# Optimization experiments

Hardware: AMD Instinct MI355X
Metric: run time of the kernel (lower is better)

The kernel has to match this reference:

```python
import jax, jax.numpy as jnp
import numpy as np

B, T, C = 4, 1024, 1024
N_HEAD = 16
MEMORY = 64  # sliding-window size: key j visible to query i iff 0 <= i-j <= MEMORY


def setup_inputs() -> dict:
    key = jax.random.key(0)
    k1, k2, k3 = jax.random.split(key, 3)
    x = jax.random.normal(k1, (B, T, C), dtype=jnp.float32)
    # torch Linear weight is [out, in]; we store transposed [in, out] for x @ W
    W_attn = jax.random.normal(k2, (C, 3 * C), dtype=jnp.float32) * (1.0 / np.sqrt(C))
    W_proj = jax.random.normal(k3, (C, C), dtype=jnp.float32) * (1.0 / np.sqrt(C))
    return {"x": x, "W_attn": W_attn, "W_proj": W_proj}


def reference(x, W_attn, W_proj):
    Bv, Tv, Cv = x.shape
    hd = Cv // N_HEAD
    qkv = x @ W_attn                               # [B,T,3C]
    q, k, v = jnp.split(qkv, 3, axis=-1)
    def heads(t):
        return t.reshape(Bv, Tv, N_HEAD, hd).transpose(0, 2, 1, 3)  # [B,H,T,hd]
    q, k, v = heads(q), heads(k), heads(v)
    scale = 1.0 / np.sqrt(hd)
    scores = jnp.einsum('bhqd,bhkd->bhqk', q, k) * scale            # [B,H,T,T]
    i = jnp.arange(Tv)
    diff = i[:, None] - i[None, :]                                  # i - j
    band_mask = (diff >= 0) & (diff <= MEMORY)                      # M1 * ~M2
    y = jax.nn.softmax(jnp.where(band_mask, scores, -jnp.inf), axis=-1) @ v
    # get_att=True path: full causal attention probabilities (no window)
    att = jax.nn.softmax(jnp.where(diff >= 0, scores, -jnp.inf), axis=-1)
    att_std = jnp.std(att, axis=0, ddof=1)                          # torch .std default ddof=1
    y = y.transpose(0, 2, 1, 3).reshape(Bv, Tv, Cv)
    y = y @ W_proj
    return (y, att, att_std)
```

## Files before the change

kernel.cpp:

```cpp
#include <hip/hip_runtime.h>
#include <hip/hip_bf16.h>
#include <stdint.h>

#define Bb 4
#define Tt 1024
#define Hh 16
#define HD 64
#define C3 3072
#define WIN 64

typedef __bf16 bf16x8 __attribute__((ext_vector_type(8)));
typedef float f32x4 __attribute__((ext_vector_type(4)));

#define MFMA16(a, b, c) __builtin_amdgcn_mfma_f32_16x16x32_bf16((a), (b), (c), 0, 0, 0)

static __device__ __forceinline__ unsigned short f2bf(float f) {
  union { float f; unsigned u; } v; v.f = f;
  unsigned r = (v.u + 0x7FFFu + ((v.u >> 16) & 1u)) >> 16;
  return (unsigned short)r;
}
static __device__ __forceinline__ float bf2f(unsigned short h) {
  union { unsigned u; float f; } v; v.u = ((unsigned)h) << 16;
  return v.f;
}

__global__ __launch_bounds__(256) void k_prep(const float* __restrict__ x,
                                              const float* __restrict__ Wa,
                                              const float* __restrict__ Wp,
                                              unsigned short* __restrict__ xbf,
                                              unsigned short* __restrict__ WtA,
                                              unsigned short* __restrict__ WtP) {
  __shared__ float tile[32][33];
  const int blk = blockIdx.x;
  const int tid = threadIdx.x;
  if (blk < 4096) {
    int i = blk * 256 + tid;
    float4 v = ((const float4*)x)[i];
    ushort4 o;
    o.x = f2bf(v.x); o.y = f2bf(v.y); o.z = f2bf(v.z); o.w = f2bf(v.w);
    ((ushort4*)xbf)[i] = o;
    return;
  }
  const float* Win; unsigned short* Wt; int N, n0, k0;
  if (blk < 7168) { int bb = blk - 4096; Win = Wa; Wt = WtA; N = 3072; n0 = (bb % 96) * 32; k0 = (bb / 96) * 32; }
  else           { int bb = blk - 7168; Win = Wp; Wt = WtP; N = 1024; n0 = (bb % 32) * 32; k0 = (bb / 32) * 32; }
  const int K = 1024;
  int tx = tid & 31, ty = tid >> 5;
  for (int r = ty; r < 32; r += 8)
    tile[r][tx] = Win[(size_t)(k0 + r) * N + n0 + tx];
  __syncthreads();
  for (int r = ty; r < 32; r += 8)
    Wt[(size_t)(n0 + r) * K + k0 + tx] = f2bf(tile[tx][r]);
}

template <int BM, int BF16_OUT, int SCALEQ>
__global__ __launch_bounds__(256) void k_gemm_bt(const unsigned short* __restrict__ A,
                                                 const unsigned short* __restrict__ Bt,
                                                 void* __restrict__ Cv, int M, int N, int K) {
  constexpr int MI = BM / 32;
  __shared__ unsigned short lds[BM * 32 + 128 * 32];
  unsigned short* as_ = lds;
  unsigned short* bs_ = lds + BM * 32;
  const int tid = threadIdx.x;
  const int m0 = blockIdx.x * BM, n0 = blockIdx.y * 128;
  const int w = tid >> 6, lane = tid & 63;
  const int wm = (w >> 1) * (BM / 2), wn = (w & 1) * 64;
  const int lrow = lane & 15, lk = lane >> 4;

  f32x4 z = {0.f, 0.f, 0.f, 0.f};
  f32x4 acc[MI][4];
#pragma unroll
  for (int i = 0; i < MI; ++i)
#pragma unroll
    for (int j = 0; j < 4; ++j) acc[i][j] = z;

  const int nk = K >> 5;
  for (int kt = 0; kt < nk; ++kt) {
    const int k0 = kt << 5;
    __syncthreads();
#pragma unroll
    for (int p = 0; p < BM / 64; ++p) {
      int seg = tid + p * 256;
      int row = seg >> 2, ks = (seg & 3) << 3;
      __builtin_amdgcn_global_load_lds(
          (__attribute__((address_space(1))) void*)(A + (size_t)(m0 + row) * K + k0 + ks),
          (__attribute__((address_space(3))) void*)(as_ + seg * 8), 16, 0, 0);
    }
#pragma unroll
    for (int p = 0; p < 2; ++p) {
      int seg = tid + p * 256;
      int row = seg >> 2, ks = (seg & 3) << 3;
      __builtin_amdgcn_global_load_lds(
          (__attribute__((address_space(1))) void*)(Bt + (size_t)(n0 + row) * K + k0 + ks),
          (__attribute__((address_space(3))) void*)(bs_ + seg * 8), 16, 0, 0);
    }
    __syncthreads();
    bf16x8 af[MI], bfr[4];
#pragma unroll
    for (int f = 0; f < MI; ++f)
      af[f] = *(const bf16x8*)(as_ + (wm + f * 16 + lrow) * 32 + lk * 8);
#pragma unroll
    for (int f = 0; f < 4; ++f)
      bfr[f] = *(const bf16x8*)(bs_ + (wn + f * 16 + lrow) * 32 + lk * 8);
#pragma unroll
    for (int i = 0; i < MI; ++i)
#pragma unroll
      for (int j = 0; j < 4; ++j) acc[i][j] = MFMA16(af[i], bfr[j], acc[i][j]);
  }
  const int r0 = lk * 4;
#pragma unroll
  for (int i = 0; i < MI; ++i)
#pragma unroll
    for (int j = 0; j < 4; ++j)
#pragma unroll
      for (int r = 0; r < 4; ++r) {
        int gm = m0 + wm + i * 16 + r0 + r;
        int gn = n0 + wn + j * 16 + lrow;
        float v = acc[i][j][r];
        if (SCALEQ) {
          if (gn < 1024) v *= 0.125f;
        }
        if (BF16_OUT)
          ((unsigned short*)Cv)[(size_t)gm * N + gn] = f2bf(v);
        else
          ((float*)Cv)[(size_t)gm * N + gn] = v;
      }
}

__global__ __launch_bounds__(512) void k_att(const unsigned short* __restrict__ qkv,
                                             float* __restrict__ att, float* __restrict__ astd) {
  const int x = blockIdx.x;
  const int ti = (x & 1) ? (x >> 1) : (31 - (x >> 1));
  const int h = blockIdx.y;
  const int i0 = ti * 32;
  const int tid = threadIdx.x;
  const int w = tid >> 6, lane = tid & 63;
  const int lrow = lane & 15, lk = lane >> 4;

  __shared__ float smrh[2][4][32];
  __shared__ float smr[4][32];
  __shared__ float wbuf[2][8][32][36];

  {
    const int b1 = w & 3, half = w >> 2;
    const size_t qb_ = ((size_t)(b1 * Tt + i0 + lrow)) * C3 + h * 64 + lk * 8;
    bf16x8 q00 = *(const bf16x8*)(qkv + qb_);
    bf16x8 q01 = *(const bf16x8*)(qkv + qb_ + 32);
    bf16x8 q10 = *(const bf16x8*)(qkv + qb_ + (size_t)16 * C3);
    bf16x8 q11 = *(const bf16x8*)(qkv + qb_ + (size_t)16 * C3 + 32);

    float l[2][4];
#pragma unroll
    for (int i2 = 0; i2 < 2; ++i2)
#pragma unroll
      for (int r = 0; r < 4; ++r) l[i2][r] = 0.f;

    for (int jt = half; jt <= ti; jt += 2) {
      const int j0 = jt * 32;
      const size_t krowa = ((size_t)(b1 * Tt + j0 + lrow)) * C3 + 1024 + h * 64 + lk * 8;
      const size_t krowb = krowa + (size_t)16 * C3;
      bf16x8 k00 = *(const bf16x8*)(qkv + krowa);
      bf16x8 k01 = *(const bf16x8*)(qkv + krowa + 32);
      bf16x8 k10 = *(const bf16x8*)(qkv + krowb);
      bf16x8 k11 = *(const bf16x8*)(qkv + krowb + 32);
      const int ja = j0 + lrow, jb2 = j0 + 16 + lrow;
#pragma unroll
      for (int i2 = 0; i2 < 2; ++i2) {
        bf16x8 qa = i2 ? q10 : q00;
        bf16x8 qb = i2 ? q11 : q01;
        f32x4 sa = {0.f, 0.f, 0.f, 0.f}, sb = {0.f, 0.f, 0.f, 0.f};
        sa = MFMA16(qa, k00, sa);
        sa = MFMA16(qb, k01, sa);
        sb = MFMA16(qa, k10, sb);
        sb = MFMA16(qb, k11, sb);
#pragma unroll
        for (int r = 0; r < 4; ++r) {
          int ig = i0 + i2 * 16 + lk * 4 + r;
          float pa = (ja <= ig) ? __expf(sa[r]) : 0.f;
          float pb = (jb2 <= ig) ? __expf(sb[r]) : 0.f;
          l[i2][r] += pa + pb;
        }
      }
    }
#pragma unroll
    for (int i2 = 0; i2 < 2; ++i2)
#pragma unroll
      for (int r = 0; r < 4; ++r) {
        float ll = l[i2][r];
#pragma unroll
        for (int d = 1; d <= 8; d <<= 1) ll += __shfl_xor(ll, d);
        if (lrow == 0) smrh[half][b1][i2 * 16 + lk * 4 + r] = ll;
      }
  }
  __syncthreads();
  if (tid < 128) {
    int b = tid >> 5, row = tid & 31;
    smr[b][row] = 1.0f / (smrh[0][b][row] + smrh[1][b][row]);
  }
  __syncthreads();

  bf16x8 qf[4][2][2];
#pragma unroll
  for (int b = 0; b < 4; ++b) {
    const size_t qb_ = ((size_t)(b * Tt + i0 + lrow)) * C3 + h * 64 + lk * 8;
    qf[b][0][0] = *(const bf16x8*)(qkv + qb_);
    qf[b][0][1] = *(const bf16x8*)(qkv + qb_ + 32);
    qf[b][1][0] = *(const bf16x8*)(qkv + qb_ + (size_t)16 * C3);
    qf[b][1][1] = *(const bf16x8*)(qkv + qb_ + (size_t)16 * C3 + 32);
  }

  const f32x4 z4 = {0.f, 0.f, 0.f, 0.f};
  for (int jt = w; jt < 32; jt += 8) {
    const int j0 = jt * 32;
    if (jt > ti) {
#pragma unroll
      for (int b = 0; b < 4; ++b)
#pragma unroll
        for (int q = 0; q < 4; ++q) {
          int f = q * 64 + lane;
          int row = f >> 3, c4 = f & 7;
          __builtin_nontemporal_store(
              z4, (f32x4*)&att[(((size_t)(b * Hh + h)) * Tt + i0 + row) * Tt + j0 + c4 * 4]);
        }
#pragma unroll
      for (int q = 0; q < 4; ++q) {
        int f = q * 64 + lane;
        int row = f >> 3, c4 = f & 7;
        __builtin_nontemporal_store(
            z4, (f32x4*)&astd[((size_t)h * Tt + i0 + row) * Tt + j0 + c4 * 4]);
      }
      continue;
    }
    float s1[2][2][4], s2[2][2][4];
#pragma unroll
    for (int i2 = 0; i2 < 2; ++i2)
#pragma unroll
      for (int j2 = 0; j2 < 2; ++j2)
#pragma unroll
        for (int r = 0; r < 4; ++r) { s1[i2][j2][r] = 0.f; s2[i2][j2][r] = 0.f; }

#pragma unroll
    for (int b = 0; b < 4; ++b) {
      float (*wb)[36] = wbuf[b & 1][w];
      const size_t krowa = ((size_t)(b * Tt + j0 + lrow)) * C3 + 1024 + h * 64 + lk * 8;
      const size_t krowb = krowa + (size_t)16 * C3;
      bf16x8 k00 = *(const bf16x8*)(qkv + krowa);
      bf16x8 k01 = *(const bf16x8*)(qkv + krowa + 32);
      bf16x8 k10 = *(const bf16x8*)(qkv + krowb);
      bf16x8 k11 = *(const bf16x8*)(qkv + krowb + 32);
#pragma unroll
      for (int i2 = 0; i2 < 2; ++i2) {
        float rr[4];
#pragma unroll
        for (int r = 0; r < 4; ++r) rr[r] = smr[b][i2 * 16 + lk * 4 + r];
#pragma unroll
        for (int j2 = 0; j2 < 2; ++j2) {
          f32x4 s = {0.f, 0.f, 0.f, 0.f};
          s = MFMA16(qf[b][i2][0], j2 ? k10 : k00, s);
          s = MFMA16(qf[b][i2][1], j2 ? k11 : k01, s);
          const int jg2 = j0 + j2 * 16 + lrow;
#pragma unroll
          for (int r = 0; r < 4; ++r) {
            int ig = i0 + i2 * 16 + lk * 4 + r;
            float p = (jg2 <= ig) ? __expf(s[r]) * rr[r] : 0.f;
            wb[i2 * 16 + lk * 4 + r][j2 * 16 + lrow] = p;
            s1[i2][j2][r] += p;
            s2[i2][j2][r] += p * p;
          }
        }
      }
#pragma unroll
      for (int q = 0; q < 4; ++q) {
        int f = q * 64 + lane;
        int row = f >> 3, c4 = f & 7;
        f32x4 v = *(f32x4*)&wb[row][c4 * 4];
        __builtin_nontemporal_store(
            v, (f32x4*)&att[(((size_t)(b * Hh + h)) * Tt + i0 + row) * Tt + j0 + c4 * 4]);
      }
    }
#pragma unroll
    for (int i2 = 0; i2 < 2; ++i2)
#pragma unroll
      for (int j2 = 0; j2 < 2; ++j2)
#pragma unroll
        for (int r = 0; r < 4; ++r) {
          float mean = s1[i2][j2][r] * 0.25f;
          float var = (s2[i2][j2][r] - 4.f * mean * mean) * (1.f / 3.f);
          wbuf[0][w][i2 * 16 + lk * 4 + r][j2 * 16 + lrow] = sqrtf(fmaxf(var, 0.f));
        }
#pragma unroll
    for (int q = 0; q < 4; ++q) {
      int f = q * 64 + lane;
      int row = f >> 3, c4 = f & 7;
      f32x4 v = *(f32x4*)&wbuf[0][w][row][c4 * 4];
      __builtin_nontemporal_store(
          v, (f32x4*)&astd[((size_t)h * Tt + i0 + row) * Tt + j0 + c4 * 4]);
    }
  }
}

__global__ __launch_bounds__(256) void k_bandy(const unsigned short* __restrict__ qkv,
                                               unsigned short* __restrict__ yh) {
  __shared__ unsigned short qls[64 * 66];
  __shared__ unsigned short kls[128 * 66];
  __shared__ unsigned short vls[128 * 66];
  __shared__ float pls[4][80];

  int blk = blockIdx.x;
  int it = blk & 15, h = (blk >> 4) & 15, b = blk >> 8;
  int i0 = it * 64;
  int jb = i0 - 64;
  int tid = threadIdx.x;

  for (int r = tid; r < 320; r += 256) {
    unsigned short* dst;
    int grow, sel;
    if (r < 64) { dst = qls + r * 66; grow = i0 + r; sel = 0; }
    else if (r < 192) { dst = kls + (r - 64) * 66; grow = jb + (r - 64); sel = 1; }
    else { dst = vls + (r - 192) * 66; grow = jb + (r - 192); sel = 2; }
    if (grow < 0) {
      for (int t = 0; t < 32; ++t) ((unsigned*)dst)[t] = 0u;
    } else {
      const unsigned* src = (const unsigned*)(qkv + ((size_t)(b * Tt + grow)) * C3 + sel * 1024 + h * 64);
      for (int t = 0; t < 32; ++t) ((unsigned*)dst)[t] = src[t];
    }
  }
  __syncthreads();

  const int w = tid >> 6, lane = tid & 63;
  for (int rr = 0; rr < 16; ++rr) {
    const int i = i0 + (w << 4) + rr;
    const int io = i - i0;
    const int ja = i - 64 + lane;
    const unsigned* qrow = (const unsigned*)(qls + io * 66);
    const unsigned* krow = (const unsigned*)(kls + (size_t)(io + lane) * 66);
    const unsigned* kerow = (const unsigned*)(kls + (size_t)(io + 64) * 66);
    float sa = 0.f, se = 0.f;
#pragma unroll 8
    for (int t = 0; t < 32; ++t) {
      unsigned qq = qrow[t];
      float q0 = bf2f((unsigned short)qq), q1 = bf2f((unsigned short)(qq >> 16));
      unsigned kk = krow[t];
      sa = fmaf(q0, bf2f((unsigned short)kk), sa);
      sa = fmaf(q1, bf2f((unsigned short)(kk >> 16)), sa);
      unsigned ke = kerow[t];
      se = fmaf(q0, bf2f((unsigned short)ke), se);
      se = fmaf(q1, bf2f((unsigned short)(ke >> 16)), se);
    }
    if (ja < 0) sa = -1e30f;
    float m = sa;
    m = fmaxf(m, __shfl_xor(m, 1));
    m = fmaxf(m, __shfl_xor(m, 2));
    m = fmaxf(m, __shfl_xor(m, 4));
    m = fmaxf(m, __shfl_xor(m, 8));
    m = fmaxf(m, __shfl_xor(m, 16));
    m = fmaxf(m, __shfl_xor(m, 32));
    m = fmaxf(m, se);
    float pa = __expf(sa - m);
    float pe = __expf(se - m);
    float sum = pa;
    sum += __shfl_xor(sum, 1);
    sum += __shfl_xor(sum, 2);
    sum += __shfl_xor(sum, 4);
    sum += __shfl_xor(sum, 8);
    sum += __shfl_xor(sum, 16);
    sum += __shfl_xor(sum, 32);
    sum += pe;
    float rl = 1.0f / sum;
    pls[w][lane] = pa * rl;
    if (lane == 0) pls[w][64] = pe * rl;
    float y = 0.f;
#pragma unroll 4
    for (int t = 0; t <= 64; ++t)
      y = fmaf(pls[w][t], bf2f(vls[(size_t)(io + t) * 66 + lane]), y);
    yh[((size_t)(b * Tt + i)) * 1024 + h * 64 + lane] = f2bf(y);
  }
}

extern "C" void kernel_launch(void* const* d_in, const int* in_sizes, int n_in,
                              void* d_out, int out_size, void* d_ws, size_t ws_size,
                              hipStream_t stream) {
  const float* x = (const float*)d_in[0];
  const float* Wa = (const float*)d_in[1];
  const float* Wp = (const float*)d_in[2];

  float* out = (float*)d_out;
  float* y_out = out;
  float* att = out + (size_t)4194304;
  float* astd = out + (size_t)71303168;

  char* ws = (char*)d_ws;
  unsigned short* qkv = (unsigned short*)ws;
  unsigned short* yh = (unsigned short*)(ws + 25165824);
  unsigned short* WtP = (unsigned short*)(ws + 33554432);

  char* yreg = (char*)d_out;
  unsigned short* WtA = (unsigned short*)yreg;
  unsigned short* xbf = (unsigned short*)(yreg + 6291456);

  k_prep<<<8192, 256, 0, stream>>>(x, Wa, Wp, xbf, WtA, WtP);
  k_gemm_bt<128, 1, 1><<<dim3(32, 24), 256, 0, stream>>>(xbf, WtA, qkv, 4096, 3072, 1024);
  k_att<<<dim3(32, 16), 512, 0, stream>>>(qkv, att, astd);
  k_bandy<<<1024, 256, 0, stream>>>(qkv, yh);
  k_gemm_bt<64, 0, 0><<<dim3(64, 8), 256, 0, stream>>>(yh, WtP, y_out, 4096, 1024, 1024);
}
```

Before: 268.8 us.

## Write unnormalized exp scores to att, then rescale and compute std in-place

Drops the separate first pass over keys that computed the softmax denominators. Each batch's unnormalized exponentials are now written straight to the att output while row sums accumulate. After a block-wide reduction, a second pass reads att back, multiplies by the reciprocal sums, rewrites it with nontemporal stores, and computes the std across batches. This avoids a second QK^T MFMA pass and its K loads, but it re-reads and rewrites the large att tensor, adding global memory traffic on a kernel that is likely bandwidth-bound.

```diff
diff --git a/kernel.cpp b/kernel.cpp
--- a/kernel.cpp
+++ b/kernel.cpp
@@ -137,111 +137,51 @@
   const int w = tid >> 6, lane = tid & 63;
   const int lrow = lane & 15, lk = lane >> 4;
 
-  __shared__ float smrh[2][4][32];
+  __shared__ float smrh[8][4][32];
   __shared__ float smr[4][32];
   __shared__ float wbuf[2][8][32][36];
 
-  {
-    const int b1 = w & 3, half = w >> 2;
-    const size_t qb_ = ((size_t)(b1 * Tt + i0 + lrow)) * C3 + h * 64 + lk * 8;
-    bf16x8 q00 = *(const bf16x8*)(qkv + qb_);
-    bf16x8 q01 = *(const bf16x8*)(qkv + qb_ + 32);
-    bf16x8 q10 = *(const bf16x8*)(qkv + qb_ + (size_t)16 * C3);
-    bf16x8 q11 = *(const bf16x8*)(qkv + qb_ + (size_t)16 * C3 + 32);
-
-    float l[2][4];
-#pragma unroll
-    for (int i2 = 0; i2 < 2; ++i2)
-#pragma unroll
-      for (int r = 0; r < 4; ++r) l[i2][r] = 0.f;
-
-    for (int jt = half; jt <= ti; jt += 2) {
-      const int j0 = jt * 32;
-      const size_t krowa = ((size_t)(b1 * Tt + j0 + lrow)) * C3 + 1024 + h * 64 + lk * 8;
-      const size_t krowb = krowa + (size_t)16 * C3;
-      bf16x8 k00 = *(const bf16x8*)(qkv + krowa);
-      bf16x8 k01 = *(const bf16x8*)(qkv + krowa + 32);
-      bf16x8 k10 = *(const bf16x8*)(qkv + krowb);
-      bf16x8 k11 = *(const bf16x8*)(qkv + krowb + 32);
-      const int ja = j0 + lrow, jb2 = j0 + 16 + lrow;
-#pragma unroll
-      for (int i2 = 0; i2 < 2; ++i2) {
-        bf16x8 qa = i2 ? q10 : q00;
-        bf16x8 qb = i2 ? q11 : q01;
-        f32x4 sa = {0.f, 0.f, 0.f, 0.f}, sb = {0.f, 0.f, 0.f, 0.f};
-        sa = MFMA16(qa, k00, sa);
-        sa = MFMA16(qb, k01, sa);
-        sb = MFMA16(qa, k10, sb);
-        sb = MFMA16(qb, k11, sb);
-#pragma unroll
-        for (int r = 0; r < 4; ++r) {
-          int ig = i0 + i2 * 16 + lk * 4 + r;
-          float pa = (ja <= ig) ? __expf(sa[r]) : 0.f;
-          float pb = (jb2 <= ig) ? __expf(sb[r]) : 0.f;
-          l[i2][r] += pa + pb;
-        }
-      }
-    }
-#pragma unroll
-    for (int i2 = 0; i2 < 2; ++i2)
-#pragma unroll
-      for (int r = 0; r < 4; ++r) {
-        float ll = l[i2][r];
-#pragma unroll
-        for (int d = 1; d <= 8; d <<= 1) ll += __shfl_xor(ll, d);
-        if (lrow == 0) smrh[half][b1][i2 * 16 + lk * 4 + r] = ll;
-      }
-  }
-  __syncthreads();
-  if (tid < 128) {
-    int b = tid >> 5, row = tid & 31;
-    smr[b][row] = 1.0f / (smrh[0][b][row] + smrh[1][b][row]);
-  }
-  __syncthreads();
-
-  bf16x8 qf[4][2][2];
-#pragma unroll
+  const f32x4 z4 = {0.f, 0.f, 0.f, 0.f};
+
+#pragma unroll 1
   for (int b = 0; b < 4; ++b) {
     const size_t qb_ = ((size_t)(b * Tt + i0 + lrow)) * C3 + h * 64 + lk * 8;
-    qf[b][0][0] = *(const bf16x8*)(qkv + qb_);
-    qf[b][0][1] = *(const bf16x8*)(qkv + qb_ + 32);
-    qf[b][1][0] = *(const bf16x8*)(qkv + qb_ + (size_t)16 * C3);
-    qf[b][1][1] = *(const bf16x8*)(qkv + qb_ + (size_t)16 * C3 + 32);
-  }
-
-  const f32x4 z4 = {0.f, 0.f, 0.f, 0.f};
-  for (int jt = w; jt < 32; jt += 8) {
-    const int j0 = jt * 32;
-    if (jt > ti) {
-#pragma unroll
-      for (int b = 0; b < 4; ++b)
-#pragma unroll
-        for (int q = 0; q < 4; ++q) {
-          int f = q * 64 + lane;
-          int row = f >> 3, c4 = f & 7;
-          __builtin_nontemporal_store(
-              z4, (f32x4*)&att[(((size_t)(b * Hh + h)) * Tt + i0 + row) * Tt + j0 + c4 * 4]);
+    bf16x8 qf00 = *(const bf16x8*)(qkv + qb_);
+    bf16x8 qf01 = *(const bf16x8*)(qkv + qb_ + 32);
+    bf16x8 qf10 = *(const bf16x8*)(qkv + qb_ + (size_t)16 * C3);
+    bf16x8 qf11 = *(const bf16x8*)(qkv + qb_ + (size_t)16 * C3 + 32);
+    const size_t abase = ((size_t)(b * Hh + h)) * Tt;
+
+    float rs[2][4];
+#pragma unroll
+    for (int i2 = 0; i2 < 2; ++i2)
+#pragma unroll
+      for (int r = 0; r < 4; ++r) rs[i2][r] = 0.f;
+
+    for (int jt = w; jt < 32; jt += 8) {
+      const int j0 = jt * 32;
+      if (jt > ti) {
+        if (b == 0) {
+#pragma unroll
+          for (int bz = 0; bz < 4; ++bz)
+#pragma unroll
+            for (int q = 0; q < 4; ++q) {
+              int f = q * 64 + lane;
+              int row = f >> 3, c4 = f & 7;
+              __builtin_nontemporal_store(
+                  z4, (f32x4*)&att[(((size_t)(bz * Hh + h)) * Tt + i0 + row) * Tt + j0 + c4 * 4]);
+            }
+#pragma unroll
+          for (int q = 0; q < 4; ++q) {
+            int f = q * 64 + lane;
+            int row = f >> 3, c4 = f & 7;
+            __builtin_nontemporal_store(
+                z4, (f32x4*)&astd[((size_t)h * Tt + i0 + row) * Tt + j0 + c4 * 4]);
+          }
         }
-#pragma unroll
-      for (int q = 0; q < 4; ++q) {
-        int f = q * 64 + lane;
-        int row = f >> 3, c4 = f & 7;
-        __builtin_nontemporal_store(
-            z4, (f32x4*)&astd[((size_t)h * Tt + i0 + row) * Tt + j0 + c4 * 4]);
-      }
-      continue;
-    }
-    float s1[2][2][4], s2[2][2][4];
-#pragma unroll
-    for (int i2 = 0; i2 < 2; ++i2)
-#pragma unroll
-      for (int j2 = 0; j2 < 2; ++j2)
-#pragma unroll
-        for (int r = 0; r < 4; ++r) { s1[i2][j2][r] = 0.f; s2[i2][j2][r] = 0.f; }
-
-#pragma unroll
-    for (int b = 0; b < 4; ++b) {
-      float (*wb)[36] = wbuf[b & 1][w];
+        continue;
+      }
+      float (*wb)[36] = wbuf[(jt >> 3) & 1][w];
       const size_t krowa = ((size_t)(b * Tt + j0 + lrow)) * C3 + 1024 + h * 64 + lk * 8;
       const size_t krowb = krowa + (size_t)16 * C3;
       bf16x8 k00 = *(const bf16x8*)(qkv + krowa);
@@ -250,22 +190,20 @@
       bf16x8 k11 = *(const bf16x8*)(qkv + krowb + 32);
 #pragma unroll
       for (int i2 = 0; i2 < 2; ++i2) {
-        float rr[4];
-#pragma unroll
-        for (int r = 0; r < 4; ++r) rr[r] = smr[b][i2 * 16 + lk * 4 + r];
+        bf16x8 qa = i2 ? qf10 : qf00;
+        bf16x8 qb = i2 ? qf11 : qf01;
 #pragma unroll
         for (int j2 = 0; j2 < 2; ++j2) {
           f32x4 s = {0.f, 0.f, 0.f, 0.f};
-          s = MFMA16(qf[b][i2][0], j2 ? k10 : k00, s);
-          s = MFMA16(qf[b][i2][1], j2 ? k11 : k01, s);
+          s = MFMA16(qa, j2 ? k10 : k00, s);
+          s = MFMA16(qb, j2 ? k11 : k01, s);
           const int jg2 = j0 + j2 * 16 + lrow;
 #pragma unroll
           for (int r = 0; r < 4; ++r) {
             int ig = i0 + i2 * 16 + lk * 4 + r;
-            float p = (jg2 <= ig) ? __expf(s[r]) * rr[r] : 0.f;
-            wb[i2 * 16 + lk * 4 + r][j2 * 16 + lrow] = p;
-            s1[i2][j2][r] += p;
-            s2[i2][j2][r] += p * p;
+            float e = (jg2 <= ig) ? __expf(s[r]) : 0.f;
+            wb[i2 * 16 + lk * 4 + r][j2 * 16 + lrow] = e;
+            rs[i2][r] += e;
           }
         }
       }
@@ -274,27 +212,53 @@
         int f = q * 64 + lane;
         int row = f >> 3, c4 = f & 7;
         f32x4 v = *(f32x4*)&wb[row][c4 * 4];
-        __builtin_nontemporal_store(
-            v, (f32x4*)&att[(((size_t)(b * Hh + h)) * Tt + i0 + row) * Tt + j0 + c4 * 4]);
+        *(f32x4*)&att[(abase + i0 + row) * Tt + j0 + c4 * 4] = v;
       }
     }
 #pragma unroll
     for (int i2 = 0; i2 < 2; ++i2)
 #pragma unroll
-      for (int j2 = 0; j2 < 2; ++j2)
-#pragma unroll
-        for (int r = 0; r < 4; ++r) {
-          float mean = s1[i2][j2][r] * 0.25f;
-          float var = (s2[i2][j2][r] - 4.f * mean * mean) * (1.f / 3.f);
-          wbuf[0][w][i2 * 16 + lk * 4 + r][j2 * 16 + lrow] = sqrtf(fmaxf(var, 0.f));
-        }
+      for (int r = 0; r < 4; ++r) {
+        float ll = rs[i2][r];
+#pragma unroll
+        for (int d = 1; d <= 8; d <<= 1) ll += __shfl_xor(ll, d);
+        if (lrow == 0) smrh[w][b][i2 * 16 + lk * 4 + r] = ll;
+      }
+  }
+  __syncthreads();
+  if (tid < 128) {
+    int b = tid >> 5, row = tid & 31;
+    float s = 0.f;
+#pragma unroll
+    for (int ww = 0; ww < 8; ++ww) s += smrh[ww][b][row];
+    smr[b][row] = 1.0f / s;
+  }
+  __syncthreads();
+
+  for (int jt = w; jt < 32; jt += 8) {
+    if (jt > ti) continue;
+    const int j0 = jt * 32;
 #pragma unroll
     for (int q = 0; q < 4; ++q) {
       int f = q * 64 + lane;
       int row = f >> 3, c4 = f & 7;
-      f32x4 v = *(f32x4*)&wbuf[0][w][row][c4 * 4];
-      __builtin_nontemporal_store(
-          v, (f32x4*)&astd[((size_t)h * Tt + i0 + row) * Tt + j0 + c4 * 4]);
+      const size_t roff = (size_t)(i0 + row) * Tt + j0 + c4 * 4;
+      f32x4 p0 = *(f32x4*)&att[((size_t)(0 * Hh + h)) * Tt * Tt + roff] * smr[0][row];
+      f32x4 p1 = *(f32x4*)&att[((size_t)(1 * Hh + h)) * Tt * Tt + roff] * smr[1][row];
+      f32x4 p2 = *(f32x4*)&att[((size_t)(2 * Hh + h)) * Tt * Tt + roff] * smr[2][row];
+      f32x4 p3 = *(f32x4*)&att[((size_t)(3 * Hh + h)) * Tt * Tt + roff] * smr[3][row];
+      __builtin_nontemporal_store(p0, (f32x4*)&att[((size_t)(0 * Hh + h)) * Tt * Tt + roff]);
+      __builtin_nontemporal_store(p1, (f32x4*)&att[((size_t)(1 * Hh + h)) * Tt * Tt + roff]);
+      __builtin_nontemporal_store(p2, (f32x4*)&att[((size_t)(2 * Hh + h)) * Tt * Tt + roff]);
+      __builtin_nontemporal_store(p3, (f32x4*)&att[((size_t)(3 * Hh + h)) * Tt * Tt + roff]);
+      f32x4 mean = (p0 + p1 + p2 + p3) * 0.25f;
+      f32x4 var = (p0 * p0 + p1 * p1 + p2 * p2 + p3 * p3 - 4.f * mean * mean) * (1.f / 3.f);
+      f32x4 o;
+      o.x = sqrtf(fmaxf(var.x, 0.f));
+      o.y = sqrtf(fmaxf(var.y, 0.f));
+      o.z = sqrtf(fmaxf(var.z, 0.f));
+      o.w = sqrtf(fmaxf(var.w, 0.f));
+      __builtin_nontemporal_store(o, (f32x4*)&astd[(size_t)h * Tt * Tt + roff]);
     }
   }
 }
```

After: 288.7 us. 7.4% more time.

## Merge causal-attention and band-attention kernels into one interleaved launch

Applied to the files above, without the earlier changes.

The full-causal probability/std kernel and the sliding-window output kernel are combined into one launch of 1536 blocks. Every third block runs the att/std path and the other two each handle one band tile, using a shared raw smem buffer. The intent is to drop a launch boundary and let the memory-bound att writes overlap with the compute-bound band work on the same GPU. In exchange, band blocks now use 512 threads with 8 rows per wave, and every block reserves the larger shared-memory footprint, which may lower occupancy.

```diff
diff --git a/kernel.cpp b/kernel.cpp
--- a/kernel.cpp
+++ b/kernel.cpp
@@ -127,253 +127,258 @@
       }
 }
 
-__global__ __launch_bounds__(512) void k_att(const unsigned short* __restrict__ qkv,
-                                             float* __restrict__ att, float* __restrict__ astd) {
-  const int x = blockIdx.x;
-  const int ti = (x & 1) ? (x >> 1) : (31 - (x >> 1));
-  const int h = blockIdx.y;
-  const int i0 = ti * 32;
+__global__ __launch_bounds__(512) void k_attband(const unsigned short* __restrict__ qkv,
+                                                 float* __restrict__ att, float* __restrict__ astd,
+                                                 unsigned short* __restrict__ yh) {
+  __shared__ __align__(16) char smem[75264];
+  const int bid = blockIdx.x;
+  const int g = bid / 3, rsel = bid - g * 3;
   const int tid = threadIdx.x;
   const int w = tid >> 6, lane = tid & 63;
-  const int lrow = lane & 15, lk = lane >> 4;
-
-  __shared__ float smrh[2][4][32];
-  __shared__ float smr[4][32];
-  __shared__ float wbuf[2][8][32][36];
-
-  {
-    const int b1 = w & 3, half = w >> 2;
-    const size_t qb_ = ((size_t)(b1 * Tt + i0 + lrow)) * C3 + h * 64 + lk * 8;
-    bf16x8 q00 = *(const bf16x8*)(qkv + qb_);
-    bf16x8 q01 = *(const bf16x8*)(qkv + qb_ + 32);
-    bf16x8 q10 = *(const bf16x8*)(qkv + qb_ + (size_t)16 * C3);
-    bf16x8 q11 = *(const bf16x8*)(qkv + qb_ + (size_t)16 * C3 + 32);
-
-    float l[2][4];
-#pragma unroll
-    for (int i2 = 0; i2 < 2; ++i2)
-#pragma unroll
-      for (int r = 0; r < 4; ++r) l[i2][r] = 0.f;
-
-    for (int jt = half; jt <= ti; jt += 2) {
+
+  if (rsel == 0) {
+    const int x = g & 31;
+    const int ti = (x & 1) ? (x >> 1) : (31 - (x >> 1));
+    const int h = g >> 5;
+    const int i0 = ti * 32;
+    const int lrow = lane & 15, lk = lane >> 4;
+
+    float (*smrh)[4][32] = (float(*)[4][32])smem;
+    float (*smr)[32] = (float(*)[32])(smem + 1024);
+    float (*wbuf)[8][32][36] = (float(*)[8][32][36])(smem + 1536);
+
+    {
+      const int b1 = w & 3, half = w >> 2;
+      const size_t qb_ = ((size_t)(b1 * Tt + i0 + lrow)) * C3 + h * 64 + lk * 8;
+      bf16x8 q00 = *(const bf16x8*)(qkv + qb_);
+      bf16x8 q01 = *(const bf16x8*)(qkv + qb_ + 32);
+      bf16x8 q10 = *(const bf16x8*)(qkv + qb_ + (size_t)16 * C3);
+      bf16x8 q11 = *(const bf16x8*)(qkv + qb_ + (size_t)16 * C3 + 32);
+
+      float l[2][4];
+#pragma unroll
+      for (int i2 = 0; i2 < 2; ++i2)
+#pragma unroll
+        for (int r = 0; r < 4; ++r) l[i2][r] = 0.f;
+
+      for (int jt = half; jt <= ti; jt += 2) {
+        const int j0 = jt * 32;
+        const size_t krowa = ((size_t)(b1 * Tt + j0 + lrow)) * C3 + 1024 + h * 64 + lk * 8;
+        const size_t krowb = krowa + (size_t)16 * C3;
+        bf16x8 k00 = *(const bf16x8*)(qkv + krowa);
+        bf16x8 k01 = *(const bf16x8*)(qkv + krowa + 32);
+        bf16x8 k10 = *(const bf16x8*)(qkv + krowb);
+        bf16x8 k11 = *(const bf16x8*)(qkv + krowb + 32);
+        const int ja = j0 + lrow, jb2 = j0 + 16 + lrow;
+#pragma unroll
+        for (int i2 = 0; i2 < 2; ++i2) {
+          bf16x8 qa = i2 ? q10 : q00;
+          bf16x8 qb = i2 ? q11 : q01;
+          f32x4 sa = {0.f, 0.f, 0.f, 0.f}, sb = {0.f, 0.f, 0.f, 0.f};
+          sa = MFMA16(qa, k00, sa);
+          sa = MFMA16(qb, k01, sa);
+          sb = MFMA16(qa, k10, sb);
+          sb = MFMA16(qb, k11, sb);
+#pragma unroll
+          for (int r = 0; r < 4; ++r) {
+            int ig = i0 + i2 * 16 + lk * 4 + r;
+            float pa = (ja <= ig) ? __expf(sa[r]) : 0.f;
+            float pb = (jb2 <= ig) ? __expf(sb[r]) : 0.f;
+            l[i2][r] += pa + pb;
+          }
+        }
+      }
+#pragma unroll
+      for (int i2 = 0; i2 < 2; ++i2)
+#pragma unroll
+        for (int r = 0; r < 4; ++r) {
+          float ll = l[i2][r];
+#pragma unroll
+          for (int d = 1; d <= 8; d <<= 1) ll += __shfl_xor(ll, d);
+          if (lrow == 0) smrh[half][b1][i2 * 16 + lk * 4 + r] = ll;
+        }
+    }
+    __syncthreads();
+    if (tid < 128) {
+      int b = tid >> 5, row = tid & 31;
+      smr[b][row] = 1.0f / (smrh[0][b][row] + smrh[1][b][row]);
+    }
+    __syncthreads();
+
+    bf16x8 qf[4][2][2];
+#pragma unroll
+    for (int b = 0; b < 4; ++b) {
+      const size_t qb_ = ((size_t)(b * Tt + i0 + lrow)) * C3 + h * 64 + lk * 8;
+      qf[b][0][0] = *(const bf16x8*)(qkv + qb_);
+      qf[b][0][1] = *(const bf16x8*)(qkv + qb_ + 32);
+      qf[b][1][0] = *(const bf16x8*)(qkv + qb_ + (size_t)16 * C3);
+      qf[b][1][1] = *(const bf16x8*)(qkv + qb_ + (size_t)16 * C3 + 32);
+    }
+
+    const f32x4 z4 = {0.f, 0.f, 0.f, 0.f};
+    for (int jt = w; jt < 32; jt += 8) {
       const int j0 = jt * 32;
-      const size_t krowa = ((size_t)(b1 * Tt + j0 + lrow)) * C3 + 1024 + h * 64 + lk * 8;
-      const size_t krowb = krowa + (size_t)16 * C3;
-      bf16x8 k00 = *(const bf16x8*)(qkv + krowa);
-      bf16x8 k01 = *(const bf16x8*)(qkv + krowa + 32);
-      bf16x8 k10 = *(const bf16x8*)(qkv + krowb);
-      bf16x8 k11 = *(const bf16x8*)(qkv + krowb + 32);
-      const int ja = j0 + lrow, jb2 = j0 + 16 + lrow;
-#pragma unroll
-      for (int i2 = 0; i2 < 2; ++i2) {
-        bf16x8 qa = i2 ? q10 : q00;
-        bf16x8 qb = i2 ? q11 : q01;
-        f32x4 sa = {0.f, 0.f, 0.f, 0.f}, sb = {0.f, 0.f, 0.f, 0.f};
-        sa = MFMA16(qa, k00, sa);
-        sa = MFMA16(qb, k01, sa);
-        sb = MFMA16(qa, k10, sb);
-        sb = MFMA16(qb, k11, sb);
-#pragma unroll
-        for (int r = 0; r < 4; ++r) {
-          int ig = i0 + i2 * 16 + lk * 4 + r;
-          float pa = (ja <= ig) ? __expf(sa[r]) : 0.f;
-          float pb = (jb2 <= ig) ? __expf(sb[r]) : 0.f;
-          l[i2][r] += pa + pb;
-        }
-      }
-    }
-#pragma unroll
-    for (int i2 = 0; i2 < 2; ++i2)
-#pragma unroll
-      for (int r = 0; r < 4; ++r) {
-        float ll = l[i2][r];
-#pragma unroll
-        for (int d = 1; d <= 8; d <<= 1) ll += __shfl_xor(ll, d);
-        if (lrow == 0) smrh[half][b1][i2 * 16 + lk * 4 + r] = ll;
-      }
-  }
-  __syncthreads();
-  if (tid < 128) {
-    int b = tid >> 5, row = tid & 31;
-    smr[b][row] = 1.0f / (smrh[0][b][row] + smrh[1][b][row]);
-  }
-  __syncthreads();
-
-  bf16x8 qf[4][2][2];
-#pragma unroll
-  for (int b = 0; b < 4; ++b) {
-    const size_t qb_ = ((size_t)(b * Tt + i0 + lrow)) * C3 + h * 64 + lk * 8;
-    qf[b][0][0] = *(const bf16x8*)(qkv + qb_);
-    qf[b][0][1] = *(const bf16x8*)(qkv + qb_ + 32);
-    qf[b][1][0] = *(const bf16x8*)(qkv + qb_ + (size_t)16 * C3);
-    qf[b][1][1] = *(const bf16x8*)(qkv + qb_ + (size_t)16 * C3 + 32);
-  }
-
-  const f32x4 z4 = {0.f, 0.f, 0.f, 0.f};
-  for (int jt = w; jt < 32; jt += 8) {
-    const int j0 = jt * 32;
-    if (jt > ti) {
-#pragma unroll
-      for (int b = 0; b < 4; ++b)
+      if (jt > ti) {
+#pragma unroll
+        for (int b = 0; b < 4; ++b)
+#pragma unroll
+          for (int q = 0; q < 4; ++q) {
+            int f = q * 64 + lane;
+            int row = f >> 3, c4 = f & 7;
+            __builtin_nontemporal_store(
+                z4, (f32x4*)&att[(((size_t)(b * Hh + h)) * Tt + i0 + row) * Tt + j0 + c4 * 4]);
+          }
 #pragma unroll
         for (int q = 0; q < 4; ++q) {
           int f = q * 64 + lane;
           int row = f >> 3, c4 = f & 7;
           __builtin_nontemporal_store(
-              z4, (f32x4*)&att[(((size_t)(b * Hh + h)) * Tt + i0 + row) * Tt + j0 + c4 * 4]);
-        }
+              z4, (f32x4*)&astd[((size_t)h * Tt + i0 + row) * Tt + j0 + c4 * 4]);
+        }
+        continue;
+      }
+      float s1[2][2][4], s2[2][2][4];
+#pragma unroll
+      for (int i2 = 0; i2 < 2; ++i2)
+#pragma unroll
+        for (int j2 = 0; j2 < 2; ++j2)
+#pragma unroll
+          for (int r = 0; r < 4; ++r) { s1[i2][j2][r] = 0.f; s2[i2][j2][r] = 0.f; }
+
+#pragma unroll
+      for (int b = 0; b < 4; ++b) {
+        float (*wb)[36] = wbuf[b & 1][w];
+        const size_t krowa = ((size_t)(b * Tt + j0 + lrow)) * C3 + 1024 + h * 64 + lk * 8;
+        const size_t krowb = krowa + (size_t)16 * C3;
+        bf16x8 k00 = *(const bf16x8*)(qkv + krowa);
+        bf16x8 k01 = *(const bf16x8*)(qkv + krowa + 32);
+        bf16x8 k10 = *(const bf16x8*)(qkv + krowb);
+        bf16x8 k11 = *(const bf16x8*)(qkv + krowb + 32);
+#pragma unroll
+        for (int i2 = 0; i2 < 2; ++i2) {
+          float rr[4];
+#pragma unroll
+          for (int r = 0; r < 4; ++r) rr[r] = smr[b][i2 * 16 + lk * 4 + r];
+#pragma unroll
+          for (int j2 = 0; j2 < 2; ++j2) {
+            f32x4 s = {0.f, 0.f, 0.f, 0.f};
+            s = MFMA16(qf[b][i2][0], j2 ? k10 : k00, s);
+            s = MFMA16(qf[b][i2][1], j2 ? k11 : k01, s);
+            const int jg2 = j0 + j2 * 16 + lrow;
+#pragma unroll
+            for (int r = 0; r < 4; ++r) {
+              int ig = i0 + i2 * 16 + lk * 4 + r;
+              float p = (jg2 <= ig) ? __expf(s[r]) * rr[r] : 0.f;
+              wb[i2 * 16 + lk * 4 + r][j2 * 16 + lrow] = p;
+              s1[i2][j2][r] += p;
+              s2[i2][j2][r] += p * p;
+            }
+          }
+        }
+#pragma unroll
+        for (int q = 0; q < 4; ++q) {
+          int f = q * 64 + lane;
+          int row = f >> 3, c4 = f & 7;
+          f32x4 v = *(f32x4*)&wb[row][c4 * 4];
+          __builtin_nontemporal_store(
+              v, (f32x4*)&att[(((size_t)(b * Hh + h)) * Tt + i0 + row) * Tt + j0 + c4 * 4]);
+        }
+      }
+#pragma unroll
+      for (int i2 = 0; i2 < 2; ++i2)
+#pragma unroll
+        for (int j2 = 0; j2 < 2; ++j2)
+#pragma unroll
+          for (int r = 0; r < 4; ++r) {
+            float mean = s1[i2][j2][r] * 0.25f;
+            float var = (s2[i2][j2][r] - 4.f * mean * mean) * (1.f / 3.f);
+            wbuf[0][w][i2 * 16 + lk * 4 + r][j2 * 16 + lrow] = sqrtf(fmaxf(var, 0.f));
+          }
 #pragma unroll
       for (int q = 0; q < 4; ++q) {
         int f = q * 64 + lane;
         int row = f >> 3, c4 = f & 7;
+        f32x4 v = *(f32x4*)&wbuf[0][w][row][c4 * 4];
         __builtin_nontemporal_store(
-            z4, (f32x4*)&astd[((size_t)h * Tt + i0 + row) * Tt + j0 + c4 * 4]);
-      }
-      continue;
-    }
-    float s1[2][2][4], s2[2][2][4];
-#pragma unroll
-    for (int i2 = 0; i2 < 2; ++i2)
-#pragma unroll
-      for (int j2 = 0; j2 < 2; ++j2)
-#pragma unroll
-        for (int r = 0; r < 4; ++r) { s1[i2][j2][r] = 0.f; s2[i2][j2][r] = 0.f; }
-
-#pragma unroll
-    for (int b = 0; b < 4; ++b) {
-      float (*wb)[36] = wbuf[b & 1][w];
-      const size_t krowa = ((size_t)(b * Tt + j0 + lrow)) * C3 + 1024 + h * 64 + lk * 8;
-      const size_t krowb = krowa + (size_t)16 * C3;
-      bf16x8 k00 = *(const bf16x8*)(qkv + krowa);
-      bf16x8 k01 = *(const bf16x8*)(qkv + krowa + 32);
-      bf16x8 k10 = *(const bf16x8*)(qkv + krowb);
-      bf16x8 k11 = *(const bf16x8*)(qkv + krowb + 32);
-#pragma unroll
-      for (int i2 = 0; i2 < 2; ++i2) {
-        float rr[4];
-#pragma unroll
-        for (int r = 0; r < 4; ++r) rr[r] = smr[b][i2 * 16 + lk * 4 + r];
-#pragma unroll
-        for (int j2 = 0; j2 < 2; ++j2) {
-          f32x4 s = {0.f, 0.f, 0.f, 0.f};
-          s = MFMA16(qf[b][i2][0], j2 ? k10 : k00, s);
-          s = MFMA16(qf[b][i2][1], j2 ? k11 : k01, s);
-          const int jg2 = j0 + j2 * 16 + lrow;
-#pragma unroll
-          for (int r = 0; r < 4; ++r) {
-            int ig = i0 + i2 * 16 + lk * 4 + r;
-            float p = (jg2 <= ig) ? __expf(s[r]) * rr[r] : 0.f;
-            wb[i2 * 16 + lk * 4 + r][j2 * 16 + lrow] = p;
-            s1[i2][j2][r] += p;
-            s2[i2][j2][r] += p * p;
-          }
-        }
-      }
-#pragma unroll
-      for (int q = 0; q < 4; ++q) {
-        int f = q * 64 + lane;
-        int row = f >> 3, c4 = f & 7;
-        f32x4 v = *(f32x4*)&wb[row][c4 * 4];
-        __builtin_nontemporal_store(
-            v, (f32x4*)&att[(((size_t)(b * Hh + h)) * Tt + i0 + row) * Tt + j0 + c4 * 4]);
-      }
-    }
-#pragma unroll
-    for (int i2 = 0; i2 < 2; ++i2)
-#pragma unroll
-      for (int j2 = 0; j2 < 2; ++j2)
-#pragma unroll
-        for (int r = 0; r < 4; ++r) {
-          float mean = s1[i2][j2][r] * 0.25f;
-          float var = (s2[i2][j2][r] - 4.f * mean * mean) * (1.f / 3.f);
-          wbuf[0][w][i2 * 16 + lk * 4 + r][j2 * 16 + lrow] = sqrtf(fmaxf(var, 0.f));
-        }
-#pragma unroll
-    for (int q = 0; q < 4; ++q) {
-      int f = q * 64 + lane;
-      int row = f >> 3, c4 = f & 7;
-      f32x4 v = *(f32x4*)&wbuf[0][w][row][c4 * 4];
-      __builtin_nontemporal_store(
-          v, (f32x4*)&astd[((size_t)h * Tt + i0 + row) * Tt + j0 + c4 * 4]);
-    }
+            v, (f32x4*)&astd[((size_t)h * Tt + i0 + row) * Tt + j0 + c4 * 4]);
+      }
+    }
+    return;
   }
-}
-
-__global__ __launch_bounds__(256) void k_bandy(const unsigned short* __restrict__ qkv,
-                                               unsigned short* __restrict__ yh) {
-  __shared__ unsigned short qls[64 * 66];
-  __shared__ unsigned short kls[128 * 66];
-  __shared__ unsigned short vls[128 * 66];
-  __shared__ float pls[4][80];
-
-  int blk = blockIdx.x;
-  int it = blk & 15, h = (blk >> 4) & 15, b = blk >> 8;
-  int i0 = it * 64;
-  int jb = i0 - 64;
-  int tid = threadIdx.x;
-
-  for (int r = tid; r < 320; r += 256) {
-    unsigned short* dst;
-    int grow, sel;
-    if (r < 64) { dst = qls + r * 66; grow = i0 + r; sel = 0; }
-    else if (r < 192) { dst = kls + (r - 64) * 66; grow = jb + (r - 64); sel = 1; }
-    else { dst = vls + (r - 192) * 66; grow = jb + (r - 192); sel = 2; }
-    if (grow < 0) {
-      for (int t = 0; t < 32; ++t) ((unsigned*)dst)[t] = 0u;
-    } else {
-      const unsigned* src = (const unsigned*)(qkv + ((size_t)(b * Tt + grow)) * C3 + sel * 1024 + h * 64);
-      for (int t = 0; t < 32; ++t) ((unsigned*)dst)[t] = src[t];
-    }
-  }
-  __syncthreads();
-
-  const int w = tid >> 6, lane = tid & 63;
-  for (int rr = 0; rr < 16; ++rr) {
-    const int i = i0 + (w << 4) + rr;
-    const int io = i - i0;
-    const int ja = i - 64 + lane;
-    const unsigned* qrow = (const unsigned*)(qls + io * 66);
-    const unsigned* krow = (const unsigned*)(kls + (size_t)(io + lane) * 66);
-    const unsigned* kerow = (const unsigned*)(kls + (size_t)(io + 64) * 66);
-    float sa = 0.f, se = 0.f;
+
+  {
+    const int blk = 2 * g + (rsel - 1);
+    unsigned short* qls = (unsigned short*)smem;
+    unsigned short* kls = qls + 64 * 66;
+    unsigned short* vls = kls + 128 * 66;
+    float (*pls)[80] = (float(*)[80])(smem + (64 + 128 + 128) * 66 * 2);
+
+    int it = blk & 15, h = (blk >> 4) & 15, b = blk >> 8;
+    int i0 = it * 64;
+    int jb = i0 - 64;
+
+    for (int r = tid; r < 320; r += 512) {
+      unsigned short* dst;
+      int grow, sel;
+      if (r < 64) { dst = qls + r * 66; grow = i0 + r; sel = 0; }
+      else if (r < 192) { dst = kls + (r - 64) * 66; grow = jb + (r - 64); sel = 1; }
+      else { dst = vls + (r - 192) * 66; grow = jb + (r - 192); sel = 2; }
+      if (grow < 0) {
+        for (int t = 0; t < 32; ++t) ((unsigned*)dst)[t] = 0u;
+      } else {
+        const unsigned* src = (const unsigned*)(qkv + ((size_t)(b * Tt + grow)) * C3 + sel * 1024 + h * 64);
+        for (int t = 0; t < 32; ++t) ((unsigned*)dst)[t] = src[t];
+      }
+    }
+    __syncthreads();
+
+    for (int rr = 0; rr < 8; ++rr) {
+      const int i = i0 + (w << 3) + rr;
+      const int io = i - i0;
+      const int ja = i - 64 + lane;
+      const unsigned* qrow = (const unsigned*)(qls + io * 66);
+      const unsigned* krow = (const unsigned*)(kls + (size_t)(io + lane) * 66);
+      const unsigned* kerow = (const unsigned*)(kls + (size_t)(io + 64) * 66);
+      float sa = 0.f, se = 0.f;
 #pragma unroll 8
-    for (int t = 0; t < 32; ++t) {
-      unsigned qq = qrow[t];
-      float q0 = bf2f((unsigned short)qq), q1 = bf2f((unsigned short)(qq >> 16));
-      unsigned kk = krow[t];
-      sa = fmaf(q0, bf2f((unsigned short)kk), sa);
-      sa = fmaf(q1, bf2f((unsigned short)(kk >> 16)), sa);
-      unsigned ke = kerow[t];
-      se = fmaf(q0, bf2f((unsigned short)ke), se);
-      se = fmaf(q1, bf2f((unsigned short)(ke >> 16)), se);
-    }
-    if (ja < 0) sa = -1e30f;
-    float m = sa;
-    m = fmaxf(m, __shfl_xor(m, 1));
-    m = fmaxf(m, __shfl_xor(m, 2));
-    m = fmaxf(m, __shfl_xor(m, 4));
-    m = fmaxf(m, __shfl_xor(m, 8));
-    m = fmaxf(m, __shfl_xor(m, 16));
-    m = fmaxf(m, __shfl_xor(m, 32));
-    m = fmaxf(m, se);
-    float pa = __expf(sa - m);
-    float pe = __expf(se - m);
-    float sum = pa;
-    sum += __shfl_xor(sum, 1);
-    sum += __shfl_xor(sum, 2);
-    sum += __shfl_xor(sum, 4);
-    sum += __shfl_xor(sum, 8);
-    sum += __shfl_xor(sum, 16);
-    sum += __shfl_xor(sum, 32);
-    sum += pe;
-    float rl = 1.0f / sum;
-    pls[w][lane] = pa * rl;
-    if (lane == 0) pls[w][64] = pe * rl;
-    float y = 0.f;
+      for (int t = 0; t < 32; ++t) {
+        unsigned qq = qrow[t];
+        float q0 = bf2f((unsigned short)qq), q1 = bf2f((unsigned short)(qq >> 16));
+        unsigned kk = krow[t];
+        sa = fmaf(q0, bf2f((unsigned short)kk), sa);
+        sa = fmaf(q1, bf2f((unsigned short)(kk >> 16)), sa);
+        unsigned ke = kerow[t];
+        se = fmaf(q0, bf2f((unsigned short)ke), se);
+        se = fmaf(q1, bf2f((unsigned short)(ke >> 16)), se);
+      }
+      if (ja < 0) sa = -1e30f;
+      float m = sa;
+      m = fmaxf(m, __shfl_xor(m, 1));
+      m = fmaxf(m, __shfl_xor(m, 2));
+      m = fmaxf(m, __shfl_xor(m, 4));
+      m = fmaxf(m, __shfl_xor(m, 8));
+      m = fmaxf(m, __shfl_xor(m, 16));
+      m = fmaxf(m, __shfl_xor(m, 32));
+      m = fmaxf(m, se);
+      float pa = __expf(sa - m);
+      float pe = __expf(se - m);
+      float sum = pa;
+      sum += __shfl_xor(sum, 1);
+      sum += __shfl_xor(sum, 2);
+      sum += __shfl_xor(sum, 4);
+      sum += __shfl_xor(sum, 8);
+      sum += __shfl_xor(sum, 16);
+      sum += __shfl_xor(sum, 32);
+      sum += pe;
+      float rl = 1.0f / sum;
+      pls[w][lane] = pa * rl;
+      if (lane == 0) pls[w][64] = pe * rl;
+      float y = 0.f;
 #pragma unroll 4
-    for (int t = 0; t <= 64; ++t)
-      y = fmaf(pls[w][t], bf2f(vls[(size_t)(io + t) * 66 + lane]), y);
-    yh[((size_t)(b * Tt + i)) * 1024 + h * 64 + lane] = f2bf(y);
+      for (int t = 0; t <= 64; ++t)
+        y = fmaf(pls[w][t], bf2f(vls[(size_t)(io + t) * 66 + lane]), y);
+      yh[((size_t)(b * Tt + i)) * 1024 + h * 64 + lane] = f2bf(y);
+    }
   }
 }
 
@@ -400,7 +405,6 @@
 
   k_prep<<<8192, 256, 0, stream>>>(x, Wa, Wp, xbf, WtA, WtP);
   k_gemm_bt<128, 1, 1><<<dim3(32, 24), 256, 0, stream>>>(xbf, WtA, qkv, 4096, 3072, 1024);
-  k_att<<<dim3(32, 16), 512, 0, stream>>>(qkv, att, astd);
-  k_bandy<<<1024, 256, 0, stream>>>(qkv, yh);
+  k_attband<<<1536, 512, 0, stream>>>(qkv, att, astd, yh);
   k_gemm_bt<64, 0, 0><<<dim3(64, 8), 256, 0, stream>>>(yh, WtP, y_out, 4096, 1024, 1024);
 }
```

After: 262.7 us (median of 2 runs). 2.3% less time.
